# Kernel tuning notes

Measured on AMD Instinct MI355X. Metric: run time of the kernel, lower is better.

The kernel has to match this reference:

```python
import jax, jax.numpy as jnp
import numpy as np

OBS, PRED = 8, 12
E, H, G = 64, 128, 8
NEIGH = 2.0
B, P = 32, 32
N = B * P


def setup_inputs():
    key = jax.random.key(0)
    ks = jax.random.split(key, 16)

    def u(k, shape, fan_in):
        lim = 1.0 / np.sqrt(fan_in)
        return jax.random.uniform(k, shape, jnp.float32, -lim, lim)

    d_in = E + H + E  # input to each LSTM gate: [emb, h, social]
    starts = jnp.arange(B, dtype=jnp.int32) * P
    return {
        "obs_traj_rel": jax.random.normal(ks[0], (OBS, N, 2), jnp.float32) * 0.3,
        "obs_traj": jax.random.normal(ks[1], (OBS, N, 2), jnp.float32),
        "seq_start_end": jnp.stack([starts, starts + P], axis=1),
        "We": u(ks[2], (2, E), 2), "be": u(ks[3], (E,), 2),
        "Wp": u(ks[4], (H * G * G, E), H * G * G), "bp": u(ks[5], (E,), H * G * G),
        "Wi": u(ks[6], (d_in, H), d_in), "bi": u(ks[7], (H,), d_in),
        "Wf": u(ks[8], (d_in, H), d_in), "bf": u(ks[9], (H,), d_in),
        "Wo": u(ks[10], (d_in, H), d_in), "bo": u(ks[11], (H,), d_in),
        "Wg": u(ks[12], (d_in, H), d_in), "bg": u(ks[13], (H,), d_in),
        "Wout": u(ks[14], (H, 2), H), "bout": u(ks[15], (2,), H),
    }


def _social_pool(hid, pos, Wp, bp, nb):
    # hid [N,H], pos [N,2]; sequences are contiguous, equal-size blocks of P peds.
    n, h_dim = hid.shape
    p = n // nb
    hb = hid.reshape(nb, p, h_dim)
    pb = pos.reshape(nb, p, 2)
    rel = pb[:, None, :, :] - pb[:, :, None, :]          # [B, Pi, Pj, 2]
    gnorm = NEIGH / (G - 1)
    relc = jnp.clip(rel / gnorm, -(G // 2), G // 2)
    grid = (relc + G // 2).astype(jnp.int32)             # trunc == floor (vals >= 0)
    gx, gy = grid[..., 0], grid[..., 1]
    eye = jnp.eye(p, dtype=bool)[None]
    valid = (gx >= 0) & (gx < G) & (gy >= 0) & (gy < G) & (~eye)
    bins = gy * G + gx                                    # flat (y, x) bin, matches [y][x] layout
    onehot = jax.nn.one_hot(bins, G * G, dtype=hid.dtype) * valid[..., None]
    pooled = jnp.einsum('bijk,bjh->bikh', onehot, hb)     # [B, P, G*G, H] scatter-add
    flat = pooled.reshape(n, G * G * h_dim)
    return jax.nn.relu(flat @ Wp + bp)


def _cell(x, h_prev, c_prev, s, Wi, bi, Wf, bf, Wo, bo, Wg, bg):
    comb = jnp.concatenate([x, h_prev, s], axis=1)
    i = jax.nn.sigmoid(comb @ Wi + bi)
    f = jax.nn.sigmoid(comb @ Wf + bf)
    o = jax.nn.sigmoid(comb @ Wo + bo)
    g = jnp.tanh(comb @ Wg + bg)
    c = f * c_prev + i * g
    return o * jnp.tanh(c), c


def reference(obs_traj_rel, obs_traj, seq_start_end, We, be, Wp, bp,
              Wi, bi, Wf, bf, Wo, bo, Wg, bg, Wout, bout):
    n = obs_traj_rel.shape[1]
    nb = seq_start_end.shape[0]
    h = jnp.zeros((n, H), obs_traj_rel.dtype)
    c = jnp.zeros((n, H), obs_traj_rel.dtype)
    curr_pos = obs_traj[-1]
    for t in range(OBS):
        emb = obs_traj_rel[t] @ We + be
        curr_pos = obs_traj[t]
        s = _social_pool(h, curr_pos, Wp, bp, nb)
        h, c = _cell(emb, h, c, s, Wi, bi, Wf, bf, Wo, bo, Wg, bg)
    preds = []
    for _ in range(PRED):
        s = _social_pool(h, curr_pos, Wp, bp, nb)
        pv = h @ Wout + bout
        curr_pos = curr_pos + pv
        preds.append(pv)
        emb = pv @ We + be
        h, c = _cell(emb, h, c, s, Wi, bi, Wf, bf, Wo, bo, Wg, bg)
    return jnp.stack(preds, axis=0)  # [pred_len, num_peds, 2]
```

## Files before the change

kernel.cpp:

```cpp
#include <hip/hip_runtime.h>

typedef short s8v __attribute__((ext_vector_type(8)));
typedef float f32x4 __attribute__((ext_vector_type(4)));

#define OBS_T 8
#define NSTEPS 20

__device__ __forceinline__ unsigned short f2bf(float x) {
    unsigned u = __float_as_uint(x);
    u = (u + 0x7FFFu + ((u >> 16) & 1u)) >> 16;
    return (unsigned short)u;
}
__device__ __forceinline__ float bf2f(unsigned short h) {
    return __uint_as_float(((unsigned)h) << 16);
}
__device__ __forceinline__ void store2(unsigned short* H, unsigned short* M,
                                       int ci, float v) {
    unsigned short h = f2bf(v);
    H[ci] = h; M[ci] = f2bf(v - bf2f(h));
}

__global__ void slstm_prep(const float* __restrict__ Wp,
                           const float* __restrict__ Wi, const float* __restrict__ Wf,
                           const float* __restrict__ Wo, const float* __restrict__ Wg,
                           unsigned short* __restrict__ W4H, unsigned short* __restrict__ W4L,
                           unsigned short* __restrict__ WpH, unsigned short* __restrict__ WpL) {
    int x = blockIdx.x * blockDim.x + threadIdx.x;
    const int NW4 = 32 * 8 * 64 * 8;
    const int NWP = 64 * 4 * 4 * 64 * 8;
    if (x < NW4) {
        int j = x & 7, lane = (x >> 3) & 63, ks = (x >> 9) & 7, nt2 = x >> 12;
        int q = nt2 & 3, wvb = nt2 >> 2;
        int col = wvb * 16 + (lane & 15);
        int k = ks * 32 + ((lane >> 4) << 3) + j;
        const float* W = (q == 0) ? Wi : (q == 1) ? Wf : (q == 2) ? Wo : Wg;
        float v = W[k * 128 + col];
        unsigned short h = f2bf(v);
        W4H[x] = h; W4L[x] = f2bf(v - bf2f(h));
    } else if (x < NW4 + NWP) {
        int y = x - NW4;
        int j = y & 7, lane = (y >> 3) & 63, ks = (y >> 9) & 3, nt = (y >> 11) & 3, bin = y >> 13;
        int e = nt * 16 + (lane & 15);
        int k = ks * 32 + ((lane >> 4) << 3) + j;
        float v = Wp[(bin * 128 + k) * 64 + e];
        unsigned short h = f2bf(v);
        WpH[y] = h; WpL[y] = f2bf(v - bf2f(h));
    }
}

struct SP {
    const float *obs_rel, *obs_abs, *We, *be, *bp, *bi, *bfv, *bo, *bg, *Wout, *bout;
    const unsigned short *W4H, *W4L, *WpH, *WpL;
    unsigned short *hBH, *hBM;
    float *hFG, *cG, *posG;
    unsigned char *ulG;
    unsigned *jneedG;
    int *nUG;
    unsigned short *glistG;
    unsigned long long *gstartG;
    float *YG;
    float *out;
};

__global__ __launch_bounds__(512, 2) void slstm_socialY(SP p) {
    const int seq = blockIdx.x & 31;
    const int wrole = blockIdx.x >> 5;
    const int tid = threadIdx.x, lane = tid & 63, wv = tid >> 6;
    const int W = wrole * 8 + wv;
    const int slotG = W >> 2;
    const int jhalf = (W >> 1) & 1;
    const int np = W & 1;
    const int arow = jhalf * 16 + (lane & 15);
    const int j4 = (lane >> 4) << 2;
    const unsigned short* hH = p.hBH + (size_t)seq * 4096;
    const unsigned short* hM = p.hBM + (size_t)seq * 4096;
    float* Yb = p.YG + (size_t)seq * 131072;
    const int nU = p.nUG[seq];

    s8v Ah[4], Am[4];
#pragma unroll
    for (int ks = 0; ks < 4; ++ks) {
        int o = arow * 128 + ks * 32 + ((lane >> 4) << 3);
        Ah[ks] = *(const s8v*)&hH[o];
        Am[ks] = *(const s8v*)&hM[o];
    }
    for (int slot = slotG; slot < nU; slot += 16) {
        int bin = p.ulG[seq * 64 + slot];
        unsigned halfmask = (p.jneedG[seq * 64 + bin] >> (16 * jhalf)) & 0xFFFFu;
        if (!halfmask) continue;
        s8v bh0[4], bl0[4], bh1[4], bl1[4];
#pragma unroll
        for (int ks = 0; ks < 4; ++ks) {
            int foA = ((bin * 4 + np * 2) * 4 + ks) * 64 + lane;
            int foB = ((bin * 4 + np * 2 + 1) * 4 + ks) * 64 + lane;
            bh0[ks] = ((const s8v*)p.WpH)[foA];
            bl0[ks] = ((const s8v*)p.WpL)[foA];
            bh1[ks] = ((const s8v*)p.WpH)[foB];
            bl1[ks] = ((const s8v*)p.WpL)[foB];
        }
        f32x4 a0 = {0.f, 0.f, 0.f, 0.f};
        f32x4 a1 = {0.f, 0.f, 0.f, 0.f};
#pragma unroll
        for (int ks = 0; ks < 4; ++ks) {
            a0 = __builtin_amdgcn_mfma_f32_16x16x32_bf16(Am[ks], bh0[ks], a0, 0, 0, 0);
            a0 = __builtin_amdgcn_mfma_f32_16x16x32_bf16(Ah[ks], bl0[ks], a0, 0, 0, 0);
            a0 = __builtin_amdgcn_mfma_f32_16x16x32_bf16(Ah[ks], bh0[ks], a0, 0, 0, 0);
            a1 = __builtin_amdgcn_mfma_f32_16x16x32_bf16(Am[ks], bh1[ks], a1, 0, 0, 0);
            a1 = __builtin_amdgcn_mfma_f32_16x16x32_bf16(Ah[ks], bl1[ks], a1, 0, 0, 0);
            a1 = __builtin_amdgcn_mfma_f32_16x16x32_bf16(Ah[ks], bh1[ks], a1, 0, 0, 0);
        }
#pragma unroll
        for (int nt = 0; nt < 2; ++nt) {
            int e = (np * 2 + nt) * 16 + (lane & 15);
            const f32x4 a = nt ? a1 : a0;
#pragma unroll
            for (int r = 0; r < 4; ++r) {
                if ((halfmask >> (j4 + r)) & 1u) {
                    int j = jhalf * 16 + j4 + r;
                    Yb[(slot * 32 + j) * 64 + e] = a[r];
                }
            }
        }
    }
}

__global__ __launch_bounds__(512, 1) void slstm_step(SP p, int t) {
    __shared__ __align__(16) unsigned short combH[32 * 256];
    __shared__ __align__(16) unsigned short combM[32 * 256];
    __shared__ float posb[64];
    __shared__ float pvbuf[64];
    __shared__ float red[256];
    __shared__ unsigned char binTabL[1024];
    __shared__ unsigned char binSlotL[64];
    __shared__ unsigned jneedS[64];
    __shared__ float biasL[512], beL[64], bpL[64], WeL[128], WoutL[256], boutL[2];

    const int seq = blockIdx.x;
    const int tid = threadIdx.x;
    const int lane = tid & 63;
    const int wv = tid >> 6;
    const int gi = tid >> 4;
    const int gg = tid & 15;
    const int hc = wv * 16 + (lane & 15);
    const float gnorm = (float)(2.0 / 7.0);

    if (tid < 512) biasL[tid] = (tid < 128) ? p.bi[tid] : (tid < 256) ? p.bfv[tid - 128]
                              : (tid < 384) ? p.bo[tid - 256] : p.bg[tid - 384];
    if (tid < 64) { beL[tid] = p.be[tid]; bpL[tid] = p.bp[tid]; }
    if (tid < 128) WeL[tid] = p.We[tid];
    if (tid < 256) WoutL[tid] = p.Wout[tid];
    if (tid < 2) boutL[tid] = p.bout[tid];

    if (t > 0) {
        for (int x = tid; x < 4096; x += 512) {
            int row = x >> 7, k = x & 127;
            int ci = row * 256 + ((64 + k) ^ ((row & 7) << 3));
            combH[ci] = p.hBH[seq * 4096 + x];
            combM[ci] = p.hBM[seq * 4096 + x];
        }
    } else {
        for (int x = tid; x < 4096; x += 512) {
            int row = x >> 7, k = x & 127;
            int ci = row * 256 + ((64 + k) ^ ((row & 7) << 3));
            combH[ci] = 0; combM[ci] = 0;
        }
    }
    __syncthreads();

    float sreg[4] = {0.f, 0.f, 0.f, 0.f};
    if (t > 0) {
        const int e0 = gg * 4;
        const unsigned long long sp = p.gstartG[seq * 32 + gi];
        const int cnt = (int)(sp >> 40);
        const unsigned short* gl = p.glistG + seq * 1024 + gi * 32;
        const float* Yb = p.YG + (size_t)seq * 131072;
        for (int p0 = 0; p0 < cnt; p0 += 4) {
            unsigned long long e4 = *(const unsigned long long*)&gl[p0];
            int n = cnt - p0;
            unsigned en0 = (unsigned)(e4 & 0xFFFF), en1 = (unsigned)((e4 >> 16) & 0xFFFF);
            unsigned en2 = (unsigned)((e4 >> 32) & 0xFFFF), en3 = (unsigned)((e4 >> 48) & 0xFFFF);
            float4 y0, y1, y2, y3;
            if (n > 0) y0 = *(const float4*)&Yb[(((en0 >> 5) * 32) + (en0 & 31)) * 64 + e0];
            if (n > 1) y1 = *(const float4*)&Yb[(((en1 >> 5) * 32) + (en1 & 31)) * 64 + e0];
            if (n > 2) y2 = *(const float4*)&Yb[(((en2 >> 5) * 32) + (en2 & 31)) * 64 + e0];
            if (n > 3) y3 = *(const float4*)&Yb[(((en3 >> 5) * 32) + (en3 & 31)) * 64 + e0];
            if (n > 0) { sreg[0] += y0.x; sreg[1] += y0.y; sreg[2] += y0.z; sreg[3] += y0.w; }
            if (n > 1) { sreg[0] += y1.x; sreg[1] += y1.y; sreg[2] += y1.z; sreg[3] += y1.w; }
            if (n > 2) { sreg[0] += y2.x; sreg[1] += y2.y; sreg[2] += y2.z; sreg[3] += y2.w; }
            if (n > 3) { sreg[0] += y3.x; sreg[1] += y3.y; sreg[2] += y3.z; sreg[3] += y3.w; }
        }
    }
    {
        int e0 = gg * 4;
#pragma unroll
        for (int r = 0; r < 4; ++r) {
            float v = fmaxf(sreg[r] + bpL[e0 + r], 0.f);
            store2(combH, combM, gi * 256 + ((192 + e0 + r) ^ ((gi & 7) << 3)), v);
        }
    }

    if (t < OBS_T) {
        int e0 = gg * 4;
        float x0 = p.obs_rel[t * 2048 + seq * 64 + gi * 2];
        float x1 = p.obs_rel[t * 2048 + seq * 64 + gi * 2 + 1];
#pragma unroll
        for (int r = 0; r < 4; ++r) {
            int e = e0 + r;
            float v = x0 * WeL[e] + x1 * WeL[64 + e] + beL[e];
            store2(combH, combM, gi * 256 + (e ^ ((gi & 7) << 3)), v);
        }
    } else {
        if (tid < 64) posb[tid] = p.posG[seq * 64 + tid];
        if (tid < 256) {
            int i = tid >> 3, d = (tid >> 2) & 1, pp = tid & 3;
            float acc = 0.f;
            int k0 = pp * 32;
            for (int k = k0; k < k0 + 32; ++k)
                acc += p.hFG[seq * 4096 + i * 128 + k] * WoutL[k * 2 + d];
            red[tid] = acc;
        }
        __syncthreads();
        if (tid < 64) {
            int d = tid & 1;
            float pv = red[tid * 4] + red[tid * 4 + 1] + red[tid * 4 + 2] + red[tid * 4 + 3]
                     + boutL[d];
            p.out[(t - OBS_T) * 2048 + seq * 64 + tid] = pv;
            posb[tid] += pv;
            p.posG[seq * 64 + tid] = posb[tid];
            pvbuf[tid] = pv;
        }
        __syncthreads();
        {
            int e0 = gg * 4;
            float x0 = pvbuf[gi * 2], x1 = pvbuf[gi * 2 + 1];
#pragma unroll
            for (int r = 0; r < 4; ++r) {
                int e = e0 + r;
                float v = x0 * WeL[e] + x1 * WeL[64 + e] + beL[e];
                store2(combH, combM, gi * 256 + (e ^ ((gi & 7) << 3)), v);
            }
        }
    }
    __syncthreads();

    f32x4 acc[4][2];
    {
        f32x4 zero = {0.f, 0.f, 0.f, 0.f};
#pragma unroll
        for (int q = 0; q < 4; ++q) { acc[q][0] = zero; acc[q][1] = zero; }
        s8v gbh[2][4], gbl[2][4];
#pragma unroll
        for (int q = 0; q < 4; ++q) {
            int fo = ((wv * 4 + q) * 8 + 0) * 64 + lane;
            gbh[0][q] = ((const s8v*)p.W4H)[fo];
            gbl[0][q] = ((const s8v*)p.W4L)[fo];
        }
#pragma unroll
        for (int ks = 0; ks < 8; ++ks) {
            const int cb = ks & 1;
            if (ks < 7) {
#pragma unroll
                for (int q = 0; q < 4; ++q) {
                    int fo = ((wv * 4 + q) * 8 + ks + 1) * 64 + lane;
                    gbh[cb ^ 1][q] = ((const s8v*)p.W4H)[fo];
                    gbl[cb ^ 1][q] = ((const s8v*)p.W4L)[fo];
                }
            }
            s8v Ah[2], Am[2];
#pragma unroll
            for (int m = 0; m < 2; ++m) {
                int row = m * 16 + (lane & 15);
                int k = ks * 32 + ((lane >> 4) << 3);
                int ci = row * 256 + (k ^ ((row & 7) << 3));
                Ah[m] = *(const s8v*)&combH[ci];
                Am[m] = *(const s8v*)&combM[ci];
            }
#pragma unroll
            for (int q = 0; q < 4; ++q)
#pragma unroll
                for (int m = 0; m < 2; ++m) {
                    acc[q][m] = __builtin_amdgcn_mfma_f32_16x16x32_bf16(Am[m], gbh[cb][q], acc[q][m], 0, 0, 0);
                    acc[q][m] = __builtin_amdgcn_mfma_f32_16x16x32_bf16(Ah[m], gbl[cb][q], acc[q][m], 0, 0, 0);
                    acc[q][m] = __builtin_amdgcn_mfma_f32_16x16x32_bf16(Ah[m], gbh[cb][q], acc[q][m], 0, 0, 0);
                }
        }
    }

    {
        float b0 = biasL[hc], b1 = biasL[128 + hc], b2 = biasL[256 + hc], b3 = biasL[384 + hc];
#pragma unroll
        for (int m = 0; m < 2; ++m)
#pragma unroll
            for (int r = 0; r < 4; ++r) {
                int row = m * 16 + ((lane >> 4) << 2) + r;
                int gidx = seq * 4096 + row * 128 + hc;
                float cprev = (t > 0) ? p.cG[gidx] : 0.f;
                float pi = acc[0][m][r] + b0;
                float pf = acc[1][m][r] + b1;
                float po = acc[2][m][r] + b2;
                float pg = acc[3][m][r] + b3;
                float ig = 1.f / (1.f + expf(-pi));
                float fg = 1.f / (1.f + expf(-pf));
                float og = 1.f / (1.f + expf(-po));
                float gv = tanhf(pg);
                float cv = fg * cprev + ig * gv;
                p.cG[gidx] = cv;
                float hv = og * tanhf(cv);
                p.hFG[gidx] = hv;
                unsigned short hh = f2bf(hv);
                float r1 = hv - bf2f(hh);
                p.hBH[gidx] = hh;
                p.hBM[gidx] = f2bf(r1);
            }
    }

    if (t < NSTEPS - 1) {
        if (t + 1 < OBS_T) {
            if (tid < 64) posb[tid] = p.obs_abs[(t + 1) * 2048 + seq * 64 + tid];
        } else if (t + 1 == OBS_T) {
            if (tid < 64) {
                float v = p.obs_abs[7 * 2048 + seq * 64 + tid];
                posb[tid] = v;
                p.posG[seq * 64 + tid] = v;
            }
        }
        if (tid < 64) jneedS[tid] = 0u;
        __syncthreads();
#pragma unroll
        for (int pp = 0; pp < 2; ++pp) {
            int pr = tid + pp * 512;
            int i = pr >> 5, j = pr & 31;
            float rx = (posb[j * 2]     - posb[i * 2])     / gnorm;
            float ry = (posb[j * 2 + 1] - posb[i * 2 + 1]) / gnorm;
            rx = fminf(fmaxf(rx, -4.f), 4.f);
            ry = fminf(fmaxf(ry, -4.f), 4.f);
            int gx = (int)(rx + 4.f);
            int gy = (int)(ry + 4.f);
            int valid = (gx < 8) && (gy < 8) && (i != j);
            int bin = gy * 8 + gx;
            binTabL[pr] = valid ? (unsigned char)bin : (unsigned char)255;
            if (valid) atomicOr(&jneedS[bin], 1u << j);
        }
        __syncthreads();
        if (wv == 0) {
            bool used = jneedS[lane] != 0u;
            unsigned long long bal = __ballot(used);
            int myIdx = __popcll(bal & ((1ull << lane) - 1ull));
            if (used) p.ulG[seq * 64 + myIdx] = (unsigned char)lane;
            binSlotL[lane] = used ? (unsigned char)myIdx : (unsigned char)255;
            if (lane == 0) p.nUG[seq] = (int)__popcll(bal);
        }
        if (tid < 64) p.jneedG[seq * 64 + tid] = jneedS[tid];
        __syncthreads();
        if (tid < 32) {
            const int i = tid;
            unsigned rw[8];
#pragma unroll
            for (int w = 0; w < 8; ++w)
                rw[w] = *(const unsigned*)&binTabL[i * 32 + w * 4];
            unsigned long long cntp = 0;
#pragma unroll
            for (int j = 0; j < 32; ++j) {
                unsigned bb = (rw[j >> 2] >> ((j & 3) * 8)) & 255u;
                if (bb != 255u) cntp += 1ull << (5 * (binSlotL[bb] >> 3));
            }
            unsigned long long pre = 0; unsigned sum = 0;
#pragma unroll
            for (int c = 0; c < 8; ++c) {
                pre |= (unsigned long long)sum << (5 * c);
                sum += (unsigned)((cntp >> (5 * c)) & 31);
            }
            p.gstartG[seq * 32 + i] = pre | ((unsigned long long)sum << 40);
            unsigned long long pos = pre;
#pragma unroll
            for (int j = 0; j < 32; ++j) {
                unsigned bb = (rw[j >> 2] >> ((j & 3) * 8)) & 255u;
                if (bb != 255u) {
                    int sg = binSlotL[bb];
                    int c = sg >> 3;
                    int pidx = (int)((pos >> (5 * c)) & 31);
                    p.glistG[seq * 1024 + i * 32 + pidx] = (unsigned short)((sg << 5) | j);
                    pos += 1ull << (5 * c);
                }
            }
        }
    }
}

__global__ __launch_bounds__(512, 1) void slstm_main_fb(
    const float* __restrict__ obs_rel, const float* __restrict__ obs_abs,
    const float* __restrict__ We, const float* __restrict__ be,
    const float* __restrict__ bp,
    const float* __restrict__ bi, const float* __restrict__ bfv,
    const float* __restrict__ bo, const float* __restrict__ bg,
    const float* __restrict__ Wout, const float* __restrict__ bout,
    const unsigned short* __restrict__ W4H, const unsigned short* __restrict__ W4L,
    const unsigned short* __restrict__ WpH, const unsigned short* __restrict__ WpL,
    float* __restrict__ out) {

    __shared__ __align__(16) unsigned short combH[32 * 256];
    __shared__ __align__(16) unsigned short combM[32 * 256];
    __shared__ __align__(16) float hbuf[32 * 128];
    __shared__ __align__(16) float scratch[32 * 512];
    __shared__ float posb[64];
    __shared__ float pvbuf[64];
    __shared__ float red[256];
    __shared__ unsigned char binTab[1024];
    __shared__ unsigned char usedList[64];
    __shared__ unsigned char binSlotG[64];
    __shared__ unsigned short glist[1024];
    __shared__ unsigned long long gstartPacked[32];
    __shared__ int nUsedS;
    __shared__ unsigned usedMask[2];
    __shared__ unsigned jm[4];
    __shared__ float biasL[512], beL[64], bpL[64], WeL[128], WoutL[256], boutL[2];

    const int tid = threadIdx.x;
    const int lane = tid & 63;
    const int wv = tid >> 6;
    const int b = blockIdx.x;

    if (tid < 512) biasL[tid] = (tid < 128) ? bi[tid] : (tid < 256) ? bfv[tid - 128]
                              : (tid < 384) ? bo[tid - 256] : bg[tid - 384];
    if (tid < 64) { beL[tid] = be[tid]; bpL[tid] = bp[tid]; }
    if (tid < 128) WeL[tid] = We[tid];
    if (tid < 256) WoutL[tid] = Wout[tid];
    if (tid < 2) boutL[tid] = bout[tid];
    for (int x = tid; x < 32 * 256; x += 512) { combH[x] = 0; combM[x] = 0; }
    for (int x = tid; x < 32 * 128; x += 512) hbuf[x] = 0.f;
    float creg[8];
#pragma unroll
    for (int r = 0; r < 8; ++r) creg[r] = 0.f;
    __syncthreads();

    const float gnorm = (float)(2.0 / 7.0);
    const int gi = tid >> 4;
    const int gg = tid & 15;
    const int hc = wv * 16 + (lane & 15);

    for (int t = 0; t < NSTEPS; ++t) {
        if (t < OBS_T) {
            if (tid < 64) posb[tid] = obs_abs[t * 2048 + b * 64 + tid];
            {
                int e0 = gg * 4;
                float x0 = obs_rel[t * 2048 + b * 64 + gi * 2];
                float x1 = obs_rel[t * 2048 + b * 64 + gi * 2 + 1];
#pragma unroll
                for (int r = 0; r < 4; ++r) {
                    int e = e0 + r;
                    float v = x0 * WeL[e] + x1 * WeL[64 + e] + beL[e];
                    store2(combH, combM, gi * 256 + (e ^ ((gi & 7) << 3)), v);
                }
            }
        }
        if (tid < 2) usedMask[tid] = 0u;
        if (tid < 4) jm[tid] = 0u;
        __syncthreads();

        float sreg[4] = {0.f, 0.f, 0.f, 0.f};
        if (t > 0) {
#pragma unroll
            for (int pp = 0; pp < 2; ++pp) {
                int p = tid + pp * 512;
                int i = p >> 5, j = p & 31;
                float rx = (posb[j * 2]     - posb[i * 2])     / gnorm;
                float ry = (posb[j * 2 + 1] - posb[i * 2 + 1]) / gnorm;
                rx = fminf(fmaxf(rx, -4.f), 4.f);
                ry = fminf(fmaxf(ry, -4.f), 4.f);
                int gx = (int)(rx + 4.f);
                int gy = (int)(ry + 4.f);
                int valid = (gx < 8) && (gy < 8) && (i != j);
                int bin = gy * 8 + gx;
                binTab[p] = valid ? (unsigned char)bin : (unsigned char)255;
                if (valid) {
                    atomicOr(&usedMask[bin >> 5], 1u << (bin & 31));
                    atomicOr(&jm[((j < 16) ? 0 : 2) + (bin >> 5)], 1u << (bin & 31));
                }
            }
            __syncthreads();
            if (wv == 0) {
                bool used = (usedMask[lane >> 5] >> (lane & 31)) & 1u;
                unsigned long long bal = __ballot(used);
                int myIdx = __popcll(bal & ((1ull << lane) - 1ull));
                if (used) { usedList[myIdx] = (unsigned char)lane; }
                binSlotG[lane] = used ? (unsigned char)myIdx : (unsigned char)255;
                if (lane == 0) nUsedS = __popcll(bal);
            }
            __syncthreads();
            const int nUsed = nUsedS;
            const int nChunks = (nUsed + 7) >> 3;

            s8v Ahs[2][4], Ams[2][4];
#pragma unroll
            for (int m = 0; m < 2; ++m)
#pragma unroll
                for (int ks = 0; ks < 4; ++ks) {
                    int row = m * 16 + (lane & 15);
                    int k = ks * 32 + ((lane >> 4) << 3);
                    int ci = row * 256 + ((64 + k) ^ ((row & 7) << 3));
                    Ahs[m][ks] = *(const s8v*)&combH[ci];
                    Ams[m][ks] = *(const s8v*)&combM[ci];
                }

            if (tid < 32) {
                const int i = tid;
                unsigned rw[8];
#pragma unroll
                for (int w = 0; w < 8; ++w)
                    rw[w] = *(const unsigned*)&binTab[i * 32 + w * 4];
                unsigned long long cntp = 0;
#pragma unroll
                for (int j = 0; j < 32; ++j) {
                    unsigned bb = (rw[j >> 2] >> ((j & 3) * 8)) & 255u;
                    if (bb != 255u) cntp += 1ull << (5 * (binSlotG[bb] >> 3));
                }
                unsigned long long pre = 0; unsigned sum = 0;
#pragma unroll
                for (int c = 0; c < 8; ++c) {
                    pre |= (unsigned long long)sum << (5 * c);
                    sum += (unsigned)((cntp >> (5 * c)) & 31);
                }
                gstartPacked[i] = pre | ((unsigned long long)sum << 40);
                unsigned long long pos = pre;
#pragma unroll
                for (int j = 0; j < 32; ++j) {
                    unsigned bb = (rw[j >> 2] >> ((j & 3) * 8)) & 255u;
                    if (bb != 255u) {
                        int sg = binSlotG[bb];
                        int c = sg >> 3;
                        int p = (int)((pos >> (5 * c)) & 31);
                        glist[i * 32 + p] = (unsigned short)((sg << 5) | j);
                        pos += 1ull << (5 * c);
                    }
                }
            }

            unsigned long long spReg = 0;
            for (int c = 0; c < nChunks; ++c) {
                int idx = c * 8 + wv;
                if (idx < nUsed) {
                    int bin = usedList[idx];
                    const bool do0 = (jm[bin >> 5]       >> (bin & 31)) & 1;
                    const bool do1 = (jm[2 + (bin >> 5)] >> (bin & 31)) & 1;
#pragma unroll
                    for (int np = 0; np < 2; ++np) {
                        s8v bh0[4], bl0[4], bh1[4], bl1[4];
#pragma unroll
                        for (int ks = 0; ks < 4; ++ks) {
                            int foA = ((bin * 4 + np * 2)     * 4 + ks) * 64 + lane;
                            int foB = ((bin * 4 + np * 2 + 1) * 4 + ks) * 64 + lane;
                            bh0[ks] = ((const s8v*)WpH)[foA];
                            bl0[ks] = ((const s8v*)WpL)[foA];
                            bh1[ks] = ((const s8v*)WpH)[foB];
                            bl1[ks] = ((const s8v*)WpL)[foB];
                        }
                        if (do0) {
                            f32x4 a0 = {0.f, 0.f, 0.f, 0.f};
                            f32x4 a1 = {0.f, 0.f, 0.f, 0.f};
#pragma unroll
                            for (int ks = 0; ks < 4; ++ks) {
                                a0 = __builtin_amdgcn_mfma_f32_16x16x32_bf16(Ams[0][ks], bh0[ks], a0, 0, 0, 0);
                                a0 = __builtin_amdgcn_mfma_f32_16x16x32_bf16(Ahs[0][ks], bl0[ks], a0, 0, 0, 0);
                                a0 = __builtin_amdgcn_mfma_f32_16x16x32_bf16(Ahs[0][ks], bh0[ks], a0, 0, 0, 0);
                                a1 = __builtin_amdgcn_mfma_f32_16x16x32_bf16(Ams[0][ks], bh1[ks], a1, 0, 0, 0);
                                a1 = __builtin_amdgcn_mfma_f32_16x16x32_bf16(Ahs[0][ks], bl1[ks], a1, 0, 0, 0);
                                a1 = __builtin_amdgcn_mfma_f32_16x16x32_bf16(Ahs[0][ks], bh1[ks], a1, 0, 0, 0);
                            }
#pragma unroll
                            for (int nt = 0; nt < 2; ++nt) {
                                int e = (np * 2 + nt) * 16 + (lane & 15);
                                const f32x4 a = nt ? a1 : a0;
#pragma unroll
                                for (int r = 0; r < 4; ++r) {
                                    int j = ((lane >> 4) << 2) + r;
                                    scratch[j * 512 + wv * 64 + (e ^ (((j >> 2) & 3) << 4))] = a[r];
                                }
                            }
                        }
                        if (do1) {
                            f32x4 a0 = {0.f, 0.f, 0.f, 0.f};
                            f32x4 a1 = {0.f, 0.f, 0.f, 0.f};
#pragma unroll
                            for (int ks = 0; ks < 4; ++ks) {
                                a0 = __builtin_amdgcn_mfma_f32_16x16x32_bf16(Ams[1][ks], bh0[ks], a0, 0, 0, 0);
                                a0 = __builtin_amdgcn_mfma_f32_16x16x32_bf16(Ahs[1][ks], bl0[ks], a0, 0, 0, 0);
                                a0 = __builtin_amdgcn_mfma_f32_16x16x32_bf16(Ahs[1][ks], bh0[ks], a0, 0, 0, 0);
                                a1 = __builtin_amdgcn_mfma_f32_16x16x32_bf16(Ams[1][ks], bh1[ks], a1, 0, 0, 0);
                                a1 = __builtin_amdgcn_mfma_f32_16x16x32_bf16(Ahs[1][ks], bl1[ks], a1, 0, 0, 0);
                                a1 = __builtin_amdgcn_mfma_f32_16x16x32_bf16(Ahs[1][ks], bh1[ks], a1, 0, 0, 0);
                            }
#pragma unroll
                            for (int nt = 0; nt < 2; ++nt) {
                                int e = (np * 2 + nt) * 16 + (lane & 15);
                                const f32x4 a = nt ? a1 : a0;
#pragma unroll
                                for (int r = 0; r < 4; ++r) {
                                    int j = 16 + ((lane >> 4) << 2) + r;
                                    scratch[j * 512 + wv * 64 + (e ^ (((j >> 2) & 3) << 4))] = a[r];
                                }
                            }
                        }
                    }
                }
                __syncthreads();
                {
                    const int e0 = gg * 4;
                    if (c == 0) spReg = gstartPacked[gi];
                    int p0 = (int)((spReg >> (5 * c)) & 31);
                    int p1 = (int)((spReg >> (5 * c + 5)) & 31);
                    for (int p = p0; p < p1; ++p) {
                        unsigned en = glist[gi * 32 + p];
                        int slot = (en >> 5) & 7;
                        int j = en & 31;
                        const float4 y = *(const float4*)
                            &scratch[j * 512 + slot * 64 + (e0 ^ (((j >> 2) & 3) << 4))];
                        sreg[0] += y.x; sreg[1] += y.y; sreg[2] += y.z; sreg[3] += y.w;
                    }
                }
                __syncthreads();
            }
        }
        {
            int e0 = gg * 4;
#pragma unroll
            for (int r = 0; r < 4; ++r) {
                float v = fmaxf(sreg[r] + bpL[e0 + r], 0.f);
                store2(combH, combM, gi * 256 + ((192 + e0 + r) ^ ((gi & 7) << 3)), v);
            }
        }
        if (t >= OBS_T) {
            if (tid < 256) {
                int i = tid >> 3, d = (tid >> 2) & 1, pp = tid & 3;
                float acc = 0.f;
                int k0 = pp * 32;
                for (int k = k0; k < k0 + 32; ++k)
                    acc += hbuf[i * 128 + (k ^ ((i & 7) << 2))] * WoutL[k * 2 + d];
                red[tid] = acc;
            }
            __syncthreads();
            if (tid < 64) {
                int d = tid & 1;
                float pv = red[tid * 4] + red[tid * 4 + 1] + red[tid * 4 + 2] + red[tid * 4 + 3]
                         + boutL[d];
                out[(t - OBS_T) * 2048 + b * 64 + tid] = pv;
                posb[tid] += pv;
                pvbuf[tid] = pv;
            }
            __syncthreads();
            {
                int e0 = gg * 4;
                float x0 = pvbuf[gi * 2], x1 = pvbuf[gi * 2 + 1];
#pragma unroll
                for (int r = 0; r < 4; ++r) {
                    int e = e0 + r;
                    float v = x0 * WeL[e] + x1 * WeL[64 + e] + beL[e];
                    store2(combH, combM, gi * 256 + (e ^ ((gi & 7) << 3)), v);
                }
            }
        }
        __syncthreads();
        {
            f32x4 acc[4][2];
            f32x4 zero = {0.f, 0.f, 0.f, 0.f};
#pragma unroll
            for (int q = 0; q < 4; ++q) { acc[q][0] = zero; acc[q][1] = zero; }
            s8v gbh[2][4], gbl[2][4];
#pragma unroll
            for (int q = 0; q < 4; ++q) {
                int fo = ((wv * 4 + q) * 8 + 0) * 64 + lane;
                gbh[0][q] = ((const s8v*)W4H)[fo];
                gbl[0][q] = ((const s8v*)W4L)[fo];
            }
#pragma unroll
            for (int ks = 0; ks < 8; ++ks) {
                const int cb = ks & 1;
                if (ks < 7) {
#pragma unroll
                    for (int q = 0; q < 4; ++q) {
                        int fo = ((wv * 4 + q) * 8 + ks + 1) * 64 + lane;
                        gbh[cb ^ 1][q] = ((const s8v*)W4H)[fo];
                        gbl[cb ^ 1][q] = ((const s8v*)W4L)[fo];
                    }
                }
                s8v Ah[2], Am[2];
#pragma unroll
                for (int m = 0; m < 2; ++m) {
                    int row = m * 16 + (lane & 15);
                    int k = ks * 32 + ((lane >> 4) << 3);
                    int ci = row * 256 + (k ^ ((row & 7) << 3));
                    Ah[m] = *(const s8v*)&combH[ci];
                    Am[m] = *(const s8v*)&combM[ci];
                }
#pragma unroll
                for (int q = 0; q < 4; ++q)
#pragma unroll
                    for (int m = 0; m < 2; ++m) {
                        acc[q][m] = __builtin_amdgcn_mfma_f32_16x16x32_bf16(Am[m], gbh[cb][q], acc[q][m], 0, 0, 0);
                        acc[q][m] = __builtin_amdgcn_mfma_f32_16x16x32_bf16(Ah[m], gbl[cb][q], acc[q][m], 0, 0, 0);
                        acc[q][m] = __builtin_amdgcn_mfma_f32_16x16x32_bf16(Ah[m], gbh[cb][q], acc[q][m], 0, 0, 0);
                    }
            }
            __syncthreads();
            float b0 = biasL[hc], b1 = biasL[128 + hc], b2 = biasL[256 + hc], b3 = biasL[384 + hc];
#pragma unroll
            for (int m = 0; m < 2; ++m)
#pragma unroll
                for (int r = 0; r < 4; ++r) {
                    int s = m * 4 + r;
                    int row = m * 16 + ((lane >> 4) << 2) + r;
                    float pi = acc[0][m][r] + b0;
                    float pf = acc[1][m][r] + b1;
                    float po = acc[2][m][r] + b2;
                    float pg = acc[3][m][r] + b3;
                    float ig = 1.f / (1.f + expf(-pi));
                    float fg = 1.f / (1.f + expf(-pf));
                    float og = 1.f / (1.f + expf(-po));
                    float gv = tanhf(pg);
                    float cv = fg * creg[s] + ig * gv;
                    creg[s] = cv;
                    float hv = og * tanhf(cv);
                    hbuf[row * 128 + (hc ^ ((row & 7) << 2))] = hv;
                    store2(combH, combM, row * 256 + ((64 + hc) ^ ((row & 7) << 3)), hv);
                }
        }
        __syncthreads();
    }
}

extern "C" void kernel_launch(void* const* d_in, const int* in_sizes, int n_in,
                              void* d_out, int out_size, void* d_ws, size_t ws_size,
                              hipStream_t stream) {
    const float* obs_rel = (const float*)d_in[0];
    const float* obs_abs = (const float*)d_in[1];
    const float* We   = (const float*)d_in[3];
    const float* be   = (const float*)d_in[4];
    const float* Wp   = (const float*)d_in[5];
    const float* bp   = (const float*)d_in[6];
    const float* Wi   = (const float*)d_in[7];
    const float* bi   = (const float*)d_in[8];
    const float* Wf   = (const float*)d_in[9];
    const float* bf   = (const float*)d_in[10];
    const float* Wo   = (const float*)d_in[11];
    const float* bo   = (const float*)d_in[12];
    const float* Wg   = (const float*)d_in[13];
    const float* bg   = (const float*)d_in[14];
    const float* Wout = (const float*)d_in[15];
    const float* bout = (const float*)d_in[16];

    char* ws = (char*)d_ws;
    unsigned short* W4H = (unsigned short*)(ws + 0);
    unsigned short* W4L = (unsigned short*)(ws + 262144);
    unsigned short* WpH = (unsigned short*)(ws + 524288);
    unsigned short* WpL = (unsigned short*)(ws + 1572864);
    unsigned short* hBH = (unsigned short*)(ws + 2621440);
    unsigned short* hBM = (unsigned short*)(ws + 2883584);
    float* hFG          = (float*)(ws + 3145728);
    float* cG           = (float*)(ws + 3670016);
    float* posG         = (float*)(ws + 4194304);
    unsigned char* ulG  = (unsigned char*)(ws + 4202496);
    unsigned* jneedG    = (unsigned*)(ws + 4204544);
    int* nUG            = (int*)(ws + 4212736);
    unsigned short* glistG = (unsigned short*)(ws + 4212992);
    unsigned long long* gstartG = (unsigned long long*)(ws + 4278528);
    float* YG           = (float*)(ws + 4286720);
    const size_t NEED   = 21063936;

    slstm_prep<<<2560, 256, 0, stream>>>(Wp, Wi, Wf, Wo, Wg, W4H, W4L, WpH, WpL);

    if (ws_size >= NEED) {
        SP p;
        p.obs_rel = obs_rel; p.obs_abs = obs_abs; p.We = We; p.be = be; p.bp = bp;
        p.bi = bi; p.bfv = bf; p.bo = bo; p.bg = bg; p.Wout = Wout; p.bout = bout;
        p.W4H = W4H; p.W4L = W4L; p.WpH = WpH; p.WpL = WpL;
        p.hBH = hBH; p.hBM = hBM; p.hFG = hFG; p.cG = cG; p.posG = posG;
        p.ulG = ulG; p.jneedG = jneedG; p.nUG = nUG;
        p.glistG = glistG; p.gstartG = gstartG; p.YG = YG; p.out = (float*)d_out;

        slstm_step<<<32, 512, 0, stream>>>(p, 0);
        for (int t = 1; t < NSTEPS; ++t) {
            slstm_socialY<<<256, 512, 0, stream>>>(p);
            slstm_step<<<32, 512, 0, stream>>>(p, t);
        }
    } else {
        slstm_main_fb<<<32, 512, 0, stream>>>(obs_rel, obs_abs, We, be, bp, bi, bf, bo, bg,
                                              Wout, bout, W4H, W4L, WpH, WpL,
                                              (float*)d_out);
    }
}
```

Baseline: 601.0 us.

## Precompute observed-step social bins in one parallel kernel, index buffers per step

Adds a kernel that computes the grid-bin tables, used-bin lists and gather lists for all observed-phase steps (t=1..8) up front, launched across 256 blocks. The bin metadata buffers are now indexed by timestep so each step kernel reads its precomputed entry. The step kernel only builds bins for the prediction phase, where positions depend on the model output. This removes serial bin building from the critical path of the observed steps, at the cost of one extra launch and a larger workspace.

Result: faster. 581.8 us (-3.2%).

```diff
diff --git a/kernel.cpp b/kernel.cpp
--- a/kernel.cpp
+++ b/kernel.cpp
@@ -62,7 +62,85 @@
     float *out;
 };
 
-__global__ __launch_bounds__(512, 2) void slstm_socialY(SP p) {
+__global__ __launch_bounds__(512, 2) void slstm_obsbins(SP p) {
+    __shared__ float posb[64];
+    __shared__ unsigned char binTabL[1024];
+    __shared__ unsigned char binSlotL[64];
+    __shared__ unsigned jneedS[64];
+
+    const int seq = blockIdx.x & 31;
+    const int tt = (blockIdx.x >> 5) + 1;
+    const int posIdx = (tt <= 7) ? tt : 7;
+    const int tid = threadIdx.x;
+    const int lane = tid & 63;
+    const int wv = tid >> 6;
+    const float gnorm = (float)(2.0 / 7.0);
+    const size_t mb = (size_t)(tt * 32 + seq);
+
+    if (tid < 64) posb[tid] = p.obs_abs[posIdx * 2048 + seq * 64 + tid];
+    if (tid < 64) jneedS[tid] = 0u;
+    __syncthreads();
+#pragma unroll
+    for (int pp = 0; pp < 2; ++pp) {
+        int pr = tid + pp * 512;
+        int i = pr >> 5, j = pr & 31;
+        float rx = (posb[j * 2]     - posb[i * 2])     / gnorm;
+        float ry = (posb[j * 2 + 1] - posb[i * 2 + 1]) / gnorm;
+        rx = fminf(fmaxf(rx, -4.f), 4.f);
+        ry = fminf(fmaxf(ry, -4.f), 4.f);
+        int gx = (int)(rx + 4.f);
+        int gy = (int)(ry + 4.f);
+        int valid = (gx < 8) && (gy < 8) && (i != j);
+        int bin = gy * 8 + gx;
+        binTabL[pr] = valid ? (unsigned char)bin : (unsigned char)255;
+        if (valid) atomicOr(&jneedS[bin], 1u << j);
+    }
+    __syncthreads();
+    if (wv == 0) {
+        bool used = jneedS[lane] != 0u;
+        unsigned long long bal = __ballot(used);
+        int myIdx = __popcll(bal & ((1ull << lane) - 1ull));
+        if (used) p.ulG[mb * 64 + myIdx] = (unsigned char)lane;
+        binSlotL[lane] = used ? (unsigned char)myIdx : (unsigned char)255;
+        if (lane == 0) p.nUG[mb] = (int)__popcll(bal);
+    }
+    if (tid < 64) p.jneedG[mb * 64 + tid] = jneedS[tid];
+    __syncthreads();
+    if (tid < 32) {
+        const int i = tid;
+        unsigned rw[8];
+#pragma unroll
+        for (int w = 0; w < 8; ++w)
+            rw[w] = *(const unsigned*)&binTabL[i * 32 + w * 4];
+        unsigned long long cntp = 0;
+#pragma unroll
+        for (int j = 0; j < 32; ++j) {
+            unsigned bb = (rw[j >> 2] >> ((j & 3) * 8)) & 255u;
+            if (bb != 255u) cntp += 1ull << (5 * (binSlotL[bb] >> 3));
+        }
+        unsigned long long pre = 0; unsigned sum = 0;
+#pragma unroll
+        for (int c = 0; c < 8; ++c) {
+            pre |= (unsigned long long)sum << (5 * c);
+            sum += (unsigned)((cntp >> (5 * c)) & 31);
+        }
+        p.gstartG[mb * 32 + i] = pre | ((unsigned long long)sum << 40);
+        unsigned long long pos = pre;
+#pragma unroll
+        for (int j = 0; j < 32; ++j) {
+            unsigned bb = (rw[j >> 2] >> ((j & 3) * 8)) & 255u;
+            if (bb != 255u) {
+                int sg = binSlotL[bb];
+                int c = sg >> 3;
+                int pidx = (int)((pos >> (5 * c)) & 31);
+                p.glistG[mb * 1024 + i * 32 + pidx] = (unsigned short)((sg << 5) | j);
+                pos += 1ull << (5 * c);
+            }
+        }
+    }
+}
+
+__global__ __launch_bounds__(512, 2) void slstm_socialY(SP p, int t) {
     const int seq = blockIdx.x & 31;
     const int wrole = blockIdx.x >> 5;
     const int tid = threadIdx.x, lane = tid & 63, wv = tid >> 6;
@@ -75,7 +153,8 @@
     const unsigned short* hH = p.hBH + (size_t)seq * 4096;
     const unsigned short* hM = p.hBM + (size_t)seq * 4096;
     float* Yb = p.YG + (size_t)seq * 131072;
-    const int nU = p.nUG[seq];
+    const size_t mb = (size_t)(t * 32 + seq);
+    const int nU = p.nUG[mb];
 
     s8v Ah[4], Am[4];
 #pragma unroll
@@ -85,8 +164,8 @@
         Am[ks] = *(const s8v*)&hM[o];
     }
     for (int slot = slotG; slot < nU; slot += 16) {
-        int bin = p.ulG[seq * 64 + slot];
-        unsigned halfmask = (p.jneedG[seq * 64 + bin] >> (16 * jhalf)) & 0xFFFFu;
+        int bin = p.ulG[mb * 64 + slot];
+        unsigned halfmask = (p.jneedG[mb * 64 + bin] >> (16 * jhalf)) & 0xFFFFu;
         if (!halfmask) continue;
         s8v bh0[4], bl0[4], bh1[4], bl1[4];
 #pragma unroll
@@ -143,6 +222,7 @@
     const int gg = tid & 15;
     const int hc = wv * 16 + (lane & 15);
     const float gnorm = (float)(2.0 / 7.0);
+    const size_t mb = (size_t)(t * 32 + seq);
 
     if (tid < 512) biasL[tid] = (tid < 128) ? p.bi[tid] : (tid < 256) ? p.bfv[tid - 128]
                               : (tid < 384) ? p.bo[tid - 256] : p.bg[tid - 384];
@@ -170,9 +250,9 @@
     float sreg[4] = {0.f, 0.f, 0.f, 0.f};
     if (t > 0) {
         const int e0 = gg * 4;
-        const unsigned long long sp = p.gstartG[seq * 32 + gi];
+        const unsigned long long sp = p.gstartG[mb * 32 + gi];
         const int cnt = (int)(sp >> 40);
-        const unsigned short* gl = p.glistG + seq * 1024 + gi * 32;
+        const unsigned short* gl = p.glistG + mb * 1024 + gi * 32;
         const float* Yb = p.YG + (size_t)seq * 131072;
         for (int p0 = 0; p0 < cnt; p0 += 4) {
             unsigned long long e4 = *(const unsigned long long*)&gl[p0];
@@ -210,7 +290,8 @@
             store2(combH, combM, gi * 256 + (e ^ ((gi & 7) << 3)), v);
         }
     } else {
-        if (tid < 64) posb[tid] = p.posG[seq * 64 + tid];
+        if (tid < 64) posb[tid] = (t == OBS_T) ? p.obs_abs[7 * 2048 + seq * 64 + tid]
+                                               : p.posG[seq * 64 + tid];
         if (tid < 256) {
             int i = tid >> 3, d = (tid >> 2) & 1, pp = tid & 3;
             float acc = 0.f;
@@ -314,16 +395,8 @@
             }
     }
 
-    if (t < NSTEPS - 1) {
-        if (t + 1 < OBS_T) {
-            if (tid < 64) posb[tid] = p.obs_abs[(t + 1) * 2048 + seq * 64 + tid];
-        } else if (t + 1 == OBS_T) {
-            if (tid < 64) {
-                float v = p.obs_abs[7 * 2048 + seq * 64 + tid];
-                posb[tid] = v;
-                p.posG[seq * 64 + tid] = v;
-            }
-        }
+    if (t >= OBS_T && t < NSTEPS - 1) {
+        const size_t nb = (size_t)((t + 1) * 32 + seq);
         if (tid < 64) jneedS[tid] = 0u;
         __syncthreads();
 #pragma unroll
@@ -346,11 +419,11 @@
             bool used = jneedS[lane] != 0u;
             unsigned long long bal = __ballot(used);
             int myIdx = __popcll(bal & ((1ull << lane) - 1ull));
-            if (used) p.ulG[seq * 64 + myIdx] = (unsigned char)lane;
+            if (used) p.ulG[nb * 64 + myIdx] = (unsigned char)lane;
             binSlotL[lane] = used ? (unsigned char)myIdx : (unsigned char)255;
-            if (lane == 0) p.nUG[seq] = (int)__popcll(bal);
-        }
-        if (tid < 64) p.jneedG[seq * 64 + tid] = jneedS[tid];
+            if (lane == 0) p.nUG[nb] = (int)__popcll(bal);
+        }
+        if (tid < 64) p.jneedG[nb * 64 + tid] = jneedS[tid];
         __syncthreads();
         if (tid < 32) {
             const int i = tid;
@@ -370,7 +443,7 @@
                 pre |= (unsigned long long)sum << (5 * c);
                 sum += (unsigned)((cntp >> (5 * c)) & 31);
             }
-            p.gstartG[seq * 32 + i] = pre | ((unsigned long long)sum << 40);
+            p.gstartG[nb * 32 + i] = pre | ((unsigned long long)sum << 40);
             unsigned long long pos = pre;
 #pragma unroll
             for (int j = 0; j < 32; ++j) {
@@ -379,7 +452,7 @@
                     int sg = binSlotL[bb];
                     int c = sg >> 3;
                     int pidx = (int)((pos >> (5 * c)) & 31);
-                    p.glistG[seq * 1024 + i * 32 + pidx] = (unsigned short)((sg << 5) | j);
+                    p.glistG[nb * 1024 + i * 32 + pidx] = (unsigned short)((sg << 5) | j);
                     pos += 1ull << (5 * c);
                 }
             }
@@ -758,12 +831,12 @@
     float* cG           = (float*)(ws + 3670016);
     float* posG         = (float*)(ws + 4194304);
     unsigned char* ulG  = (unsigned char*)(ws + 4202496);
-    unsigned* jneedG    = (unsigned*)(ws + 4204544);
-    int* nUG            = (int*)(ws + 4212736);
-    unsigned short* glistG = (unsigned short*)(ws + 4212992);
-    unsigned long long* gstartG = (unsigned long long*)(ws + 4278528);
-    float* YG           = (float*)(ws + 4286720);
-    const size_t NEED   = 21063936;
+    unsigned* jneedG    = (unsigned*)(ws + 4243456);
+    int* nUG            = (int*)(ws + 4407296);
+    unsigned long long* gstartG = (unsigned long long*)(ws + 4409856);
+    unsigned short* glistG = (unsigned short*)(ws + 4573696);
+    float* YG           = (float*)(ws + 5884416);
+    const size_t NEED   = 22661632;
 
     slstm_prep<<<2560, 256, 0, stream>>>(Wp, Wi, Wf, Wo, Wg, W4H, W4L, WpH, WpL);
 
@@ -776,9 +849,10 @@
         p.ulG = ulG; p.jneedG = jneedG; p.nUG = nUG;
         p.glistG = glistG; p.gstartG = gstartG; p.YG = YG; p.out = (float*)d_out;
 
+        slstm_obsbins<<<256, 512, 0, stream>>>(p);
         slstm_step<<<32, 512, 0, stream>>>(p, 0);
         for (int t = 1; t < NSTEPS; ++t) {
-            slstm_socialY<<<256, 512, 0, stream>>>(p);
+            slstm_socialY<<<256, 512, 0, stream>>>(p, t);
             slstm_step<<<32, 512, 0, stream>>>(p, t);
         }
     } else {
```
